# Kernel tuning notes

Hardware: AMD Instinct MI355X
Metric: run time of the kernel (lower is better)

## Reference

```python
import jax, jax.numpy as jnp
import numpy as np

NUM_HEADS = 12
D_MODEL = 768


def setup_inputs() -> dict:
    key = jax.random.key(0)
    k1, k2, k3 = jax.random.split(key, 3)
    proj_std = (2.0 / (D_MODEL + D_MODEL)) ** 0.5
    in_features = jax.random.normal(k1, (4, 2048, D_MODEL), dtype=jnp.float32)
    qkv_proj_weight = (jax.random.truncated_normal(k2, -3.0, 3.0, (3, D_MODEL, D_MODEL), dtype=jnp.float32) * proj_std)
    o_proj_weight = (jax.random.truncated_normal(k3, -3.0, 3.0, (D_MODEL, D_MODEL), dtype=jnp.float32) * proj_std)
    return {"in_features": in_features, "qkv_proj_weight": qkv_proj_weight, "o_proj_weight": o_proj_weight}


def _attention(x, qkv_w, o_w):
    b, s, d = x.shape
    h = NUM_HEADS
    dk = d // h
    # Q,K,V: x @ W^T where W is (out, in) = ((h dk), d_model)
    qkv = jnp.einsum('bsd,tod->tbso', x, qkv_w)  # (3, b, s, d)
    qkv = qkv.reshape(3, b, s, h, dk).transpose(0, 1, 3, 2, 4)  # (3, b, h, s, dk)
    Q, K, V = qkv[0], qkv[1], qkv[2]
    scores = jnp.einsum('bhqd,bhkd->bhqk', Q, K) / jnp.sqrt(jnp.float32(dk))
    causal = jnp.tril(jnp.ones((s, s), dtype=bool))
    scores = jnp.where(causal, scores, -jnp.inf)
    A = jax.nn.softmax(scores, axis=-1)
    O = jnp.einsum('bhqk,bhkd->bhqd', A, V)  # (b, h, s, dk)
    O = O.transpose(0, 2, 1, 3).reshape(b, s, d)
    return jnp.einsum('bsd,od->bso', O, o_w)


def reference(in_features, qkv_proj_weight, o_proj_weight):
    return _attention(in_features, qkv_proj_weight, o_proj_weight)
```

## Files before the change

kernel.cpp:

```cpp
#include <hip/hip_runtime.h>
#include <hip/hip_bf16.h>
#include <stdint.h>

#define SEQ 2048
#define NB 4
#define NH 12
#define DMODEL 768
#define DK 64
#define NTOK (NB*SEQ)
#define QSCALE 0.18033688011f

#define N_X4   (NTOK*DMODEL/4)
#define N_WQ4  (3*DMODEL*DMODEL/4)
#define N_WO4  (DMODEL*DMODEL/4)

typedef __bf16 bf16_t;
typedef __attribute__((ext_vector_type(4))) bf16_t bf16x4;
typedef __attribute__((ext_vector_type(8))) bf16_t bf16x8;
typedef __attribute__((ext_vector_type(4))) float f32x4;

typedef __attribute__((address_space(3))) uint32_t lds_u32_t;
typedef const __attribute__((address_space(1))) uint32_t glb_u32_t;

__device__ inline void load_lds16(const void* g, void* l) {
    __builtin_amdgcn_global_load_lds((glb_u32_t*)g, (lds_u32_t*)l, 16, 0, 0);
}

__global__ void cvt_all(const float* __restrict__ x, const float* __restrict__ wq,
                        const float* __restrict__ wo, bf16_t* __restrict__ dst) {
    int i = blockIdx.x * blockDim.x + threadIdx.x;
    const float* src; int off;
    if (i < N_X4)              { src = x;  off = i; }
    else if (i < N_X4 + N_WQ4) { src = wq; off = i - N_X4; }
    else                       { src = wo; off = i - (N_X4 + N_WQ4); }
    float4 v = ((const float4*)src)[off];
    bf16x4 o;
    o[0] = (bf16_t)v.x; o[1] = (bf16_t)v.y; o[2] = (bf16_t)v.z; o[3] = (bf16_t)v.w;
    ((bf16x4*)dst)[i] = o;
}

#define QSTAGE(AS, BS, KB) do { \
    _Pragma("unroll") \
    for (int j = 0; j < 5; j++) { \
        int c = tid + j*256; \
        if (c < 512) { \
            int row = c >> 2, cb = (c & 3) * 8; \
            load_lds16(Ap_ + (size_t)(mt*128 + row)*DMODEL + (KB) + cb, AS + c*8); \
        } else { \
            int c2 = c - 512; \
            int row = c2 >> 2, cb = (c2 & 3) * 8; \
            load_lds16(Bp_ + (size_t)(nt*192 + row)*DMODEL + (KB) + cb, BS + c2*8); \
        } \
    } \
} while (0)

#define QCOMPUTE(AS, BS) do { \
    bf16x8 af[4]; \
    _Pragma("unroll") \
    for (int f = 0; f < 4; f++) \
        af[f] = *(const bf16x8*)(AS + (wy*64 + f*16 + lr)*32 + lq*8); \
    _Pragma("unroll") \
    for (int fn = 0; fn < 6; fn++) { \
        bf16x8 bfr = *(const bf16x8*)(BS + (wx*96 + fn*16 + lr)*32 + lq*8); \
        _Pragma("unroll") \
        for (int fm = 0; fm < 4; fm++) \
            acc[fm][fn] = __builtin_amdgcn_mfma_f32_16x16x32_bf16(af[fm], bfr, acc[fm][fn], 0, 0, 0); \
    } \
} while (0)

__global__ __launch_bounds__(256, 3) void gemm_qkv(
    const bf16_t* __restrict__ Ap_, const bf16_t* __restrict__ Bp_,
    bf16_t* __restrict__ Qo, bf16_t* __restrict__ Ko, bf16_t* __restrict__ VTo)
{
    __shared__ bf16_t As0[128*32];
    __shared__ bf16_t Bs0[192*32];
    __shared__ bf16_t As1[128*32];
    __shared__ bf16_t Bs1[192*32];
    const int mt = blockIdx.x, nt = blockIdx.y;
    const int tid = threadIdx.x;
    const int w = tid >> 6, lane = tid & 63;
    const int wx = w & 1, wy = w >> 1;
    const int lr = lane & 15, lq = lane >> 4;

    f32x4 acc[4][6] = {};
    QSTAGE(As0, Bs0, 0);
    for (int kb = 0; kb < DMODEL; kb += 64) {
        __syncthreads();
        QSTAGE(As1, Bs1, kb + 32);
        QCOMPUTE(As0, Bs0);
        __syncthreads();
        if (kb + 64 < DMODEL) QSTAGE(As0, Bs0, kb + 64);
        QCOMPUTE(As1, Bs1);
    }

    const int t = nt >> 2;
    const int ob = (nt & 3) * 192 + wx * 96;
    #pragma unroll
    for (int fm = 0; fm < 4; fm++)
        #pragma unroll
        for (int fn = 0; fn < 6; fn++)
            #pragma unroll
            for (int r = 0; r < 4; r++) {
                int m = mt*128 + wy*64 + fm*16 + lq*4 + r;
                int o = ob + fn*16 + lr;
                int b = m >> 11, s = m & 2047;
                int h = o >> 6, dk = o & 63;
                float v = acc[fm][fn][r];
                if (t == 0)      Qo[(size_t)((b*NH + h)*SEQ + s)*DK + dk] = (bf16_t)(v * QSCALE);
                else if (t == 1) Ko[(size_t)((b*NH + h)*SEQ + s)*DK + dk] = (bf16_t)v;
                else             VTo[(size_t)((b*NH + h)*DK + dk)*SEQ + s] = (bf16_t)v;
            }
}

#define OSTAGE(AS, BS, KB) do { \
    _Pragma("unroll") \
    for (int j = 0; j < 3; j++) { \
        int c = tid + j*256; \
        if (c < 512) { \
            int row = c >> 2, cb = (c & 3) * 8; \
            load_lds16(Ap_ + (size_t)(mt*128 + row)*DMODEL + (KB) + cb, AS + c*8); \
        } else { \
            int c2 = c - 512; \
            int row = c2 >> 2, cb = (c2 & 3) * 8; \
            load_lds16(Bp_ + (size_t)(nt*64 + row)*DMODEL + (KB) + cb, BS + c2*8); \
        } \
    } \
} while (0)

#define OCOMPUTE(AS, BS) do { \
    bf16x8 af[4], bfr[2]; \
    _Pragma("unroll") \
    for (int f = 0; f < 4; f++) \
        af[f]  = *(const bf16x8*)(AS + (wy*64 + f*16 + lr)*32 + lq*8); \
    _Pragma("unroll") \
    for (int f = 0; f < 2; f++) \
        bfr[f] = *(const bf16x8*)(BS + (wx*32 + f*16 + lr)*32 + lq*8); \
    _Pragma("unroll") \
    for (int fm = 0; fm < 4; fm++) \
        _Pragma("unroll") \
        for (int fn = 0; fn < 2; fn++) \
            acc[fm][fn] = __builtin_amdgcn_mfma_f32_16x16x32_bf16(af[fm], bfr[fn], acc[fm][fn], 0, 0, 0); \
} while (0)

__global__ __launch_bounds__(256, 4) void gemm_oproj(
    const bf16_t* __restrict__ Ap_, const bf16_t* __restrict__ Bp_, float* __restrict__ out)
{
    __shared__ bf16_t As0[128*32];
    __shared__ bf16_t Bs0[64*32];
    __shared__ bf16_t As1[128*32];
    __shared__ bf16_t Bs1[64*32];
    const int mt = blockIdx.x, nt = blockIdx.y;
    const int tid = threadIdx.x;
    const int w = tid >> 6, lane = tid & 63;
    const int wx = w & 1, wy = w >> 1;
    const int lr = lane & 15, lq = lane >> 4;

    f32x4 acc[4][2] = {};
    OSTAGE(As0, Bs0, 0);
    for (int kb = 0; kb < DMODEL; kb += 64) {
        __syncthreads();
        OSTAGE(As1, Bs1, kb + 32);
        OCOMPUTE(As0, Bs0);
        __syncthreads();
        if (kb + 64 < DMODEL) OSTAGE(As0, Bs0, kb + 64);
        OCOMPUTE(As1, Bs1);
    }

    #pragma unroll
    for (int fm = 0; fm < 4; fm++)
        #pragma unroll
        for (int fn = 0; fn < 2; fn++)
            #pragma unroll
            for (int r = 0; r < 4; r++) {
                int m = mt*128 + wy*64 + fm*16 + lq*4 + r;
                int n = nt*64 + wx*32 + fn*16 + lr;
                out[(size_t)m*DMODEL + n] = acc[fm][fn][r];
            }
}

#define ASTAGE(KS, VS, KB) do { \
    _Pragma("unroll") \
    for (int j = 0; j < 2; j++) { \
        int rr = w*16 + j*8 + srow; \
        load_lds16(Kp + (size_t)((KB) + rr)*DK + g*8,  &KS[w*1024 + j*512 + lane*8]); \
        load_lds16(Vp + (size_t)rr*SEQ + (KB) + g*8,   &VS[w*1024 + j*512 + lane*8]); \
    } \
} while (0)

#define STRIP(A0, A1, ACC, AL, MASKED) do { \
    f32x4 sc[4]; \
    _Pragma("unroll") \
    for (int ct = 0; ct < 4; ct++) { \
        f32x4 s = {}; \
        s = __builtin_amdgcn_mfma_f32_16x16x32_bf16(A0, bk[ct][0], s, 0, 0, 0); \
        s = __builtin_amdgcn_mfma_f32_16x16x32_bf16(A1, bk[ct][1], s, 0, 0, 0); \
        sc[ct] = s; \
    } \
    _Pragma("unroll") \
    for (int ct = 0; ct < 4; ct++) \
        _Pragma("unroll") \
        for (int r = 0; r < 4; r++) { \
            float p = __builtin_amdgcn_exp2f(sc[ct][r]); \
            if (MASKED) { \
                int kl = ct*16 + lr, ql = w*16 + lq*4 + r; \
                p = (kl <= ql) ? p : 0.0f; \
            } \
            Pw[(ct>>1)*512 + (lq*4 + r + 16*((ct*2 + (lr>>3)) & 3))*8 + ((lr&7)>>1)*2 + (lr&1)] = (bf16_t)p; \
        } \
    { \
        bf16x8 ap0 = *(const bf16x8*)(Pw + lane*8); \
        bf16x8 ap1 = *(const bf16x8*)(Pw + 512 + lane*8); \
        _Pragma("unroll") \
        for (int c = 0; c < 4; c++) { \
            ACC[c] = __builtin_amdgcn_mfma_f32_16x16x32_bf16(ap0, bv[c][0], ACC[c], 0, 0, 0); \
            ACC[c] = __builtin_amdgcn_mfma_f32_16x16x32_bf16(ap1, bv[c][1], ACC[c], 0, 0, 0); \
        } \
        AL = __builtin_amdgcn_mfma_f32_16x16x32_bf16(ap0, ones, AL, 0, 0, 0); \
        AL = __builtin_amdgcn_mfma_f32_16x16x32_bf16(ap1, ones, AL, 0, 0, 0); \
    } \
} while (0)

#define AITER(KSC, VSC, KSN, VSN, T) do { \
    __syncthreads(); \
    if ((T) + 1 < nIter) ASTAGE(KSN, VSN, ((T)+1)*64); \
    bf16x8 bk[4][2], bv[4][2]; \
    const int sw = lr & 7; \
    _Pragma("unroll") \
    for (int ct = 0; ct < 4; ct++) { \
        int row = ct*16 + lr; \
        bk[ct][0] = *(const bf16x8*)(&KSC[row*64 + ((lq    ) ^ sw)*8]); \
        bk[ct][1] = *(const bf16x8*)(&KSC[row*64 + ((lq + 4) ^ sw)*8]); \
        bv[ct][0] = *(const bf16x8*)(&VSC[row*64 + ((lq    ) ^ sw)*8]); \
        bv[ct][1] = *(const bf16x8*)(&VSC[row*64 + ((lq + 4) ^ sw)*8]); \
    } \
    if ((T) <= qtA) { \
        if ((T) == qtA) { STRIP(aqA0, aqA1, accA, alA, true); } \
        else            { STRIP(aqA0, aqA1, accA, alA, false); } \
    } \
    if ((T) == nIter - 1) { STRIP(aqB0, aqB1, accB, alB, true); } \
    else                  { STRIP(aqB0, aqB1, accB, alB, false); } \
} while (0)

__global__ __launch_bounds__(256, 3) void attn(
    const bf16_t* __restrict__ Q, const bf16_t* __restrict__ K,
    const bf16_t* __restrict__ VT, bf16_t* __restrict__ O)
{
    __shared__ bf16_t Ks0[64*64];
    __shared__ bf16_t Vs0[64*64];
    __shared__ bf16_t Ks1[64*64];
    __shared__ bf16_t Vs1[64*64];
    __shared__ bf16_t P[4][1024];

    const int bh  = blockIdx.x;
    const int qtA = blockIdx.y;
    const int qtB = 31 - qtA;
    const int w = threadIdx.x >> 6, lane = threadIdx.x & 63;
    const int lr = lane & 15, lq = lane >> 4;
    const int qsA = qtA*64 + w*16;
    const int qsB = qtB*64 + w*16;
    const int srow = lane >> 3;
    const int g    = (lane & 7) ^ srow;

    const bf16_t* Qp = Q  + (size_t)bh*SEQ*DK;
    const bf16_t* Kp = K  + (size_t)bh*SEQ*DK;
    const bf16_t* Vp = VT + (size_t)bh*DK*SEQ;
    bf16_t* Pw = &P[w][0];

    const bf16x8 aqA0 = *(const bf16x8*)(Qp + (size_t)(qsA+lr)*DK + lq*8);
    const bf16x8 aqA1 = *(const bf16x8*)(Qp + (size_t)(qsA+lr)*DK + 32 + lq*8);
    const bf16x8 aqB0 = *(const bf16x8*)(Qp + (size_t)(qsB+lr)*DK + lq*8);
    const bf16x8 aqB1 = *(const bf16x8*)(Qp + (size_t)(qsB+lr)*DK + 32 + lq*8);

    bf16x8 ones;
    #pragma unroll
    for (int i = 0; i < 8; i++) ones[i] = (bf16_t)1.0f;

    f32x4 accA[4] = {}, accB[4] = {};
    f32x4 alA = {}, alB = {};

    const int nIter = 32 - qtA;

    ASTAGE(Ks0, Vs0, 0);
    int t = 0;
    while (true) {
        AITER(Ks0, Vs0, Ks1, Vs1, t); t++;
        if (t >= nIter) break;
        AITER(Ks1, Vs1, Ks0, Vs0, t); t++;
        if (t >= nIter) break;
    }

    const int b = bh / NH, h = bh % NH;
    #pragma unroll
    for (int r = 0; r < 4; r++) {
        float rlA = 1.0f / alA[r];
        float rlB = 1.0f / alB[r];
        int qa = qsA + lq*4 + r;
        int qb = qsB + lq*4 + r;
        bf16_t* opA = O + (size_t)(b*SEQ + qa)*DMODEL + h*DK;
        bf16_t* opB = O + (size_t)(b*SEQ + qb)*DMODEL + h*DK;
        #pragma unroll
        for (int c = 0; c < 4; c++) {
            opA[c*16 + lr] = (bf16_t)(accA[c][r] * rlA);
            opB[c*16 + lr] = (bf16_t)(accB[c][r] * rlB);
        }
    }
}

extern "C" void kernel_launch(void* const* d_in, const int* in_sizes, int n_in,
                              void* d_out, int out_size, void* d_ws, size_t ws_size,
                              hipStream_t stream) {
    const float* x    = (const float*)d_in[0];
    const float* wqkv = (const float*)d_in[1];
    const float* wo   = (const float*)d_in[2];
    float* out = (float*)d_out;

    char* ws = (char*)d_ws;
    const size_t SZ_X   = (size_t)NTOK*DMODEL*2;
    const size_t SZ_WQ  = (size_t)3*DMODEL*DMODEL*2;
    const size_t SZ_WO  = (size_t)DMODEL*DMODEL*2;
    const size_t SZ_HD  = (size_t)NB*NH*SEQ*DK*2;
    bf16_t* xb    = (bf16_t*)(ws);
    bf16_t* wqkvb = (bf16_t*)(ws + SZ_X);
    bf16_t* wob   = (bf16_t*)(ws + SZ_X + SZ_WQ);
    bf16_t* Qb    = (bf16_t*)(ws + SZ_X + SZ_WQ + SZ_WO);
    bf16_t* Kb    = (bf16_t*)(ws + SZ_X + SZ_WQ + SZ_WO + SZ_HD);
    bf16_t* VTb   = (bf16_t*)(ws + SZ_X + SZ_WQ + SZ_WO + 2*SZ_HD);
    bf16_t* Ob    = (bf16_t*)(ws + SZ_X + SZ_WQ + SZ_WO + 3*SZ_HD);

    cvt_all<<<(N_X4 + N_WQ4 + N_WO4) / 256, 256, 0, stream>>>(x, wqkv, wo, xb);

    gemm_qkv<<<dim3(NTOK/128, 3*DMODEL/192), 256, 0, stream>>>(xb, wqkvb, Qb, Kb, VTb);
    attn<<<dim3(NB*NH, 16), 256, 0, stream>>>(Qb, Kb, VTb, Ob);
    gemm_oproj<<<dim3(NTOK/128, DMODEL/64), 256, 0, stream>>>(Ob, wob, out);
}
```

Before: 187.8 us.

## Vectorize V^T epilogue stores and permute K rows for packed P LDS writes

The QKV projection epilogue now writes V^T as 4-wide bf16 vectors along the sequence axis instead of scattered scalar stores. In attention, K rows are loaded into LDS in a permuted order so that each lane's four score columns are contiguous. The P tile can then be written to LDS as bf16x4 packets through an XOR swizzle rather than 16 scalar bf16 stores. The causal mask index is updated to match the permutation. This adds tricky index coupling between the K permutation, the mask and the swizzle, where an error would silently break correctness.

```diff
diff --git a/kernel.cpp b/kernel.cpp
--- a/kernel.cpp
+++ b/kernel.cpp
@@ -95,21 +95,36 @@
 
     const int t = nt >> 2;
     const int ob = (nt & 3) * 192 + wx * 96;
-    #pragma unroll
-    for (int fm = 0; fm < 4; fm++)
+    if (t == 2) {
         #pragma unroll
-        for (int fn = 0; fn < 6; fn++)
+        for (int fm = 0; fm < 4; fm++)
             #pragma unroll
-            for (int r = 0; r < 4; r++) {
-                int m = mt*128 + wy*64 + fm*16 + lq*4 + r;
+            for (int fn = 0; fn < 6; fn++) {
+                int m0 = mt*128 + wy*64 + fm*16 + lq*4;
                 int o = ob + fn*16 + lr;
-                int b = m >> 11, s = m & 2047;
+                int b = m0 >> 11, s0 = m0 & 2047;
                 int h = o >> 6, dk = o & 63;
-                float v = acc[fm][fn][r];
-                if (t == 0)      Qo[(size_t)((b*NH + h)*SEQ + s)*DK + dk] = (bf16_t)(v * QSCALE);
-                else if (t == 1) Ko[(size_t)((b*NH + h)*SEQ + s)*DK + dk] = (bf16_t)v;
-                else             VTo[(size_t)((b*NH + h)*DK + dk)*SEQ + s] = (bf16_t)v;
+                bf16x4 v4;
+                #pragma unroll
+                for (int r = 0; r < 4; r++) v4[r] = (bf16_t)acc[fm][fn][r];
+                *(bf16x4*)(VTo + (size_t)((b*NH + h)*DK + dk)*SEQ + s0) = v4;
             }
+    } else {
+        #pragma unroll
+        for (int fm = 0; fm < 4; fm++)
+            #pragma unroll
+            for (int fn = 0; fn < 6; fn++)
+                #pragma unroll
+                for (int r = 0; r < 4; r++) {
+                    int m = mt*128 + wy*64 + fm*16 + lq*4 + r;
+                    int o = ob + fn*16 + lr;
+                    int b = m >> 11, s = m & 2047;
+                    int h = o >> 6, dk = o & 63;
+                    float v = acc[fm][fn][r];
+                    if (t == 0) Qo[(size_t)((b*NH + h)*SEQ + s)*DK + dk] = (bf16_t)(v * QSCALE);
+                    else        Ko[(size_t)((b*NH + h)*SEQ + s)*DK + dk] = (bf16_t)v;
+                }
+    }
 }
 
 #define OSTAGE(AS, BS, KB) do { \
@@ -182,7 +197,8 @@
     _Pragma("unroll") \
     for (int j = 0; j < 2; j++) { \
         int rr = w*16 + j*8 + srow; \
-        load_lds16(Kp + (size_t)((KB) + rr)*DK + g*8,  &KS[w*1024 + j*512 + lane*8]); \
+        int kperm = (j*8 + srow)*4 + w;   \
+        load_lds16(Kp + (size_t)((KB) + kperm)*DK + g*8,  &KS[w*1024 + j*512 + lane*8]); \
         load_lds16(Vp + (size_t)rr*SEQ + (KB) + g*8,   &VS[w*1024 + j*512 + lane*8]); \
     } \
 } while (0)
@@ -197,19 +213,22 @@
         sc[ct] = s; \
     } \
     _Pragma("unroll") \
-    for (int ct = 0; ct < 4; ct++) \
+    for (int r = 0; r < 4; r++) { \
+        bf16x4 p4; \
         _Pragma("unroll") \
-        for (int r = 0; r < 4; r++) { \
+        for (int ct = 0; ct < 4; ct++) { \
             float p = __builtin_amdgcn_exp2f(sc[ct][r]); \
             if (MASKED) { \
-                int kl = ct*16 + lr, ql = w*16 + lq*4 + r; \
+                int kl = lr*4 + ct, ql = w*16 + lq*4 + r; \
                 p = (kl <= ql) ? p : 0.0f; \
             } \
-            Pw[(ct>>1)*512 + (lq*4 + r + 16*((ct*2 + (lr>>3)) & 3))*8 + ((lr&7)>>1)*2 + (lr&1)] = (bf16_t)p; \
+            p4[ct] = (bf16_t)p; \
         } \
+        *(bf16x4*)(Pw + ((((lr>>3)*512 + (lq*4 + r + 16*((lr>>1)&3))*8 + (lr&1)*4)) ^ (((lr>>1)&3) << 4))) = p4; \
+    } \
     { \
-        bf16x8 ap0 = *(const bf16x8*)(Pw + lane*8); \
-        bf16x8 ap1 = *(const bf16x8*)(Pw + 512 + lane*8); \
+        bf16x8 ap0 = *(const bf16x8*)(Pw + ((lane ^ (lq<<1))*8)); \
+        bf16x8 ap1 = *(const bf16x8*)(Pw + 512 + ((lane ^ (lq<<1))*8)); \
         _Pragma("unroll") \
         for (int c = 0; c < 4; c++) { \
             ACC[c] = __builtin_amdgcn_mfma_f32_16x16x32_bf16(ap0, bv[c][0], ACC[c], 0, 0, 0); \
```

Result: faster. 179.9 us (-4.2%).
